# Kernel tuning notes

Hardware: AMD Instinct MI355X
Metric: run time of the kernel (lower is better)

## Reference

```python
import jax, jax.numpy as jnp
import numpy as np

N = 50000      # nodes
E = 800000     # edges (before self-loops)
NFEAT = 128
NHID = 32
H = 8
NCLASS = 47
NEG_SLOPE = 0.2  # PyG GATv2Conv default


def gatv2_layer(x, src, dst, Wl, Wr, att, b, n):
    """One GATv2Conv layer (concat over heads). att: [H, C]."""
    h, c = att.shape
    xl = (x @ Wl).reshape(n, h, c)  # source transform (lin_l)
    xr = (x @ Wr).reshape(n, h, c)  # target transform (lin_r)
    e = jax.nn.leaky_relu(xl[src] + xr[dst], NEG_SLOPE)   # [E, H, C]
    logits = jnp.einsum('ehc,hc->eh', e, att)             # [E, H]
    # segment softmax over incoming edges of each target node
    m = jax.ops.segment_max(logits, dst, num_segments=n)  # [N, H]
    alpha = jnp.exp(logits - m[dst])
    denom = jax.ops.segment_sum(alpha, dst, num_segments=n)
    alpha = alpha / (denom[dst] + 1e-16)
    msg = xl[src] * alpha[:, :, None]                     # [E, H, C]
    out = jax.ops.segment_sum(msg, dst, num_segments=n)   # [N, H, C]
    return out.reshape(n, h * c) + b


def setup_inputs():
    key = jax.random.key(0)
    ks = jax.random.split(key, 16)
    s = 0.1
    x = jax.random.normal(ks[0], (N, NFEAT), jnp.float32)
    edge_index = jax.random.randint(ks[1], (2, E), 0, N)
    HID = H * NHID  # 256
    params = dict(
        Wl0=jax.random.normal(ks[2], (NFEAT, HID), jnp.float32) * s,
        Wr0=jax.random.normal(ks[3], (NFEAT, HID), jnp.float32) * s,
        a0=jax.random.normal(ks[4], (H, NHID), jnp.float32) * s,
        b0=jnp.zeros((HID,), jnp.float32),
        Wl1=jax.random.normal(ks[5], (HID, HID), jnp.float32) * s,
        Wr1=jax.random.normal(ks[6], (HID, HID), jnp.float32) * s,
        a1=jax.random.normal(ks[7], (H, NHID), jnp.float32) * s,
        b1=jnp.zeros((HID,), jnp.float32),
        Wl2=jax.random.normal(ks[8], (HID, NCLASS), jnp.float32) * s,
        Wr2=jax.random.normal(ks[9], (HID, NCLASS), jnp.float32) * s,
        a2=jax.random.normal(ks[10], (1, NCLASS), jnp.float32) * s,
        b2=jnp.zeros((NCLASS,), jnp.float32),
    )
    return {"x": x, "edge_index": edge_index, **params}


def reference(x, edge_index, Wl0, Wr0, a0, b0, Wl1, Wr1, a1, b1, Wl2, Wr2, a2, b2):
    n = x.shape[0]
    # PyG GATv2Conv adds self-loops by default
    loops = jnp.arange(n, dtype=edge_index.dtype)
    src = jnp.concatenate([edge_index[0], loops])
    dst = jnp.concatenate([edge_index[1], loops])
    h = gatv2_layer(x, src, dst, Wl0, Wr0, a0, b0, n)
    h = jax.nn.elu(h)
    h = gatv2_layer(h, src, dst, Wl1, Wr1, a1, b1, n)
    h = jax.nn.elu(h)
    h = gatv2_layer(h, src, dst, Wl2, Wr2, a2, b2, n)
    return jax.nn.log_softmax(h, axis=-1)
```

## Files before the change

### kernel.cpp

```cpp
#include <hip/hip_runtime.h>
#include <cmath>


#define NFEAT 128
#define HID 256
#define NCLS 47
#define L2PAD 64
#define LOG2E 1.44269504088896340736f

typedef __attribute__((ext_vector_type(8))) short bf16x8;
typedef __attribute__((ext_vector_type(4))) float f32x4;
typedef __attribute__((ext_vector_type(2))) float f32x2;

__device__ __forceinline__ unsigned short f2b(float f) {
  unsigned int u = __builtin_bit_cast(unsigned int, f);
  u += 0x7FFFu + ((u >> 16) & 1u);
  return (unsigned short)(u >> 16);
}
__device__ __forceinline__ float b2f(unsigned short s) {
  return __builtin_bit_cast(float, (unsigned int)s << 16);
}
__device__ __forceinline__ f32x2 b2f2(unsigned int u) {
  return (f32x2){__builtin_bit_cast(float, u << 16),
                 __builtin_bit_cast(float, u & 0xFFFF0000u)};
}
__device__ __forceinline__ void glds16(const unsigned short* g, unsigned short* l) {
  __builtin_amdgcn_global_load_lds(
      (const __attribute__((address_space(1))) unsigned int*)g,
      (__attribute__((address_space(3))) unsigned int*)l, 16, 0, 0);
}

__global__ void k_cast_bf16(const float* __restrict__ in,
                            unsigned short* __restrict__ out, int n4) {
  int i = blockIdx.x * blockDim.x + threadIdx.x;
  if (i < n4) {
    float4 v = reinterpret_cast<const float4*>(in)[i];
    ushort4 o = {f2b(v.x), f2b(v.y), f2b(v.z), f2b(v.w)};
    reinterpret_cast<ushort4*>(out)[i] = o;
  }
}

struct WtArgs {
  const float* W[6];
  unsigned short* WT[6];
  int K[6], M[6], off[6], total;
  const float* att;
  float* att48;
};
__global__ void k_wt_all(WtArgs a) {
  int i = blockIdx.x * blockDim.x + threadIdx.x;
  if (i >= a.total) {
    int j = i - a.total;
    if (j < 48) a.att48[j] = (j < NCLS) ? a.att[j] * LOG2E : 0.f;
    return;
  }
  int s = 0;
  #pragma unroll
  for (int j = 1; j < 6; ++j) if (i >= a.off[j]) s = j;
  int jj = i - a.off[s];
  int K = a.K[s], M = a.M[s];
  int m = jj / K, k = jj - m * K;
  a.WT[s][jj] = (m < M) ? f2b(a.W[s][(size_t)k * M + m]) : (unsigned short)0;
}

__global__ void k_init_deg(int* __restrict__ deg, int n) {
  int i = blockIdx.x * blockDim.x + threadIdx.x;
  if (i < n) deg[i] = 1;
}

__global__ void k_count(const int* __restrict__ dst, int* __restrict__ deg, int e) {
  int i = blockIdx.x * blockDim.x + threadIdx.x;
  if (i < e) atomicAdd(&deg[dst[i]], 1);
}

__global__ __launch_bounds__(256) void k_bsum(const int* __restrict__ deg,
                                              int* __restrict__ bsum, int n) {
  int t = threadIdx.x;
  int base = blockIdx.x * 1024 + t * 4;
  int s = 0;
  if (base + 3 < n) {
    int4 v = *reinterpret_cast<const int4*>(deg + base);
    s = v.x + v.y + v.z + v.w;
  } else {
    for (int j = 0; j < 4; ++j) { int i = base + j; if (i < n) s += deg[i]; }
  }
  #pragma unroll
  for (int off = 1; off < 64; off <<= 1) s += __shfl_xor(s, off, 64);
  __shared__ int wsum[4];
  if ((t & 63) == 0) wsum[t >> 6] = s;
  __syncthreads();
  if (t == 0) bsum[blockIdx.x] = wsum[0] + wsum[1] + wsum[2] + wsum[3];
}

__global__ void k_scanb(int* __restrict__ bsum, int nb) {
  int lane = threadIdx.x;
  int v = (lane < nb) ? bsum[lane] : 0;
  #pragma unroll
  for (int off = 1; off < 64; off <<= 1) {
    int u = __shfl_up(v, off, 64);
    if (lane >= off) v += u;
  }
  if (lane < nb) bsum[lane] = v;
}

__global__ __launch_bounds__(256) void k_scanfinal(const int* __restrict__ deg,
                                                   const int* __restrict__ bscan,
                                                   int* __restrict__ rowptr,
                                                   int* __restrict__ adj,
                                                   int* __restrict__ vdst,
                                                   int* __restrict__ cursor, int n) {
  int t = threadIdx.x, b = blockIdx.x;
  int base = b * 1024 + t * 4;
  int v0 = 0, v1 = 0, v2 = 0, v3 = 0;
  if (base + 3 < n) {
    int4 v = *reinterpret_cast<const int4*>(deg + base);
    v0 = v.x; v1 = v.y; v2 = v.z; v3 = v.w;
  } else {
    if (base < n) v0 = deg[base];
    if (base + 1 < n) v1 = deg[base + 1];
    if (base + 2 < n) v2 = deg[base + 2];
    if (base + 3 < n) v3 = deg[base + 3];
  }
  int s = v0 + v1 + v2 + v3;
  int incl = s;
  #pragma unroll
  for (int off = 1; off < 64; off <<= 1) {
    int u = __shfl_up(incl, off, 64);
    if ((t & 63) >= off) incl += u;
  }
  __shared__ int wsum[4];
  int w = t >> 6, l = t & 63;
  if (l == 63) wsum[w] = incl;
  __syncthreads();
  int woff = 0;
  for (int j = 0; j < w; ++j) woff += wsum[j];
  int excl = incl - s + woff;
  int boff = (b == 0) ? 0 : bscan[b - 1];
  int p0 = boff + excl;
  int p1 = p0 + v0, p2 = p1 + v1, p3 = p2 + v2, p4 = p3 + v3;
  if (base < n)     { rowptr[base + 1] = p1; adj[p0] = base;     vdst[p0] = base;     cursor[base]     = p0 + 1; }
  if (base + 1 < n) { rowptr[base + 2] = p2; adj[p1] = base + 1; vdst[p1] = base + 1; cursor[base + 1] = p1 + 1; }
  if (base + 2 < n) { rowptr[base + 3] = p3; adj[p2] = base + 2; vdst[p2] = base + 2; cursor[base + 2] = p2 + 1; }
  if (base + 3 < n) { rowptr[base + 4] = p4; adj[p3] = base + 3; vdst[p3] = base + 3; cursor[base + 3] = p3 + 1; }
  if (b == 0 && t == 0) rowptr[0] = 0;
}

__global__ void k_scatter(const int* __restrict__ src, const int* __restrict__ dst,
                          int* __restrict__ cursor, int* __restrict__ adj,
                          int* __restrict__ vdst, int e) {
  int i = blockIdx.x * blockDim.x + threadIdx.x;
  if (i < e) {
    int d = dst[i];
    int p = atomicAdd(&cursor[d], 1);
    adj[p] = src[i];
    vdst[p] = d;
  }
}

__global__ __launch_bounds__(512) void gemm_dual_bf16_128(
    const unsigned short* __restrict__ X, const unsigned short* __restrict__ WlT,
    const unsigned short* __restrict__ WrT, unsigned short* __restrict__ XL,
    unsigned short* __restrict__ XR, int N, int K, int Mpad) {
  __shared__ __align__(16) unsigned short S[3 * 128 * 64];
  unsigned short* Xs = S;
  unsigned short* Ls = S + 8192;
  unsigned short* Rs = S + 16384;

  const int t = threadIdx.x;
  const int col0 = blockIdx.x * 128;
  const int row0 = blockIdx.y * 128;
  const int w = t >> 6, lane = t & 63;
  const int wr = w >> 2, wc = w & 3;
  const int r15 = lane & 15, kc = lane >> 4;
  const bool tail = (row0 + 128 > N);

  const int row_a = t >> 3,          c16_a = t & 7;
  const int row_b = (t + 512) >> 3,  c16_b = t & 7;
  const int sg_a = (c16_a ^ (row_a & 7)) * 8;
  const int sg_b = (c16_b ^ (row_b & 7)) * 8;
  unsigned short* d0 = S + w * 512;
  unsigned short* d1 = S + 4096 + w * 512;

  f32x4 accL[4][2], accR[4][2];
  #pragma unroll
  for (int rf = 0; rf < 4; ++rf)
    #pragma unroll
    for (int cf = 0; cf < 2; ++cf) {
      accL[rf][cf] = (f32x4){0.f, 0.f, 0.f, 0.f};
      accR[rf][cf] = (f32x4){0.f, 0.f, 0.f, 0.f};
    }

  for (int k0 = 0; k0 < K; k0 += 64) {
    glds16(WlT + (size_t)(col0 + row_a) * K + k0 + sg_a, d0 + 8192);
    glds16(WlT + (size_t)(col0 + row_b) * K + k0 + sg_b, d1 + 8192);
    glds16(WrT + (size_t)(col0 + row_a) * K + k0 + sg_a, d0 + 16384);
    glds16(WrT + (size_t)(col0 + row_b) * K + k0 + sg_b, d1 + 16384);
    if (!tail) {
      glds16(X + (size_t)(row0 + row_a) * K + k0 + sg_a, d0);
      glds16(X + (size_t)(row0 + row_b) * K + k0 + sg_b, d1);
    } else {
      uint4 va = (uint4){0, 0, 0, 0}, vb = (uint4){0, 0, 0, 0};
      if (row0 + row_a < N)
        va = *reinterpret_cast<const uint4*>(X + (size_t)(row0 + row_a) * K + k0 + sg_a);
      if (row0 + row_b < N)
        vb = *reinterpret_cast<const uint4*>(X + (size_t)(row0 + row_b) * K + k0 + sg_b);
      *reinterpret_cast<uint4*>(Xs + row_a * 64 + c16_a * 8) = va;
      *reinterpret_cast<uint4*>(Xs + row_b * 64 + c16_b * 8) = vb;
    }
    __syncthreads();

    #pragma unroll
    for (int ks = 0; ks < 2; ++ks) {
      const int c16 = ks * 4 + kc;
      bf16x8 a[4];
      #pragma unroll
      for (int rf = 0; rf < 4; ++rf) {
        const int rA = wr * 64 + rf * 16 + r15;
        a[rf] = *reinterpret_cast<const bf16x8*>(Xs + rA * 64 + ((c16 ^ (rA & 7)) * 8));
      }
      #pragma unroll
      for (int cf = 0; cf < 2; ++cf) {
        const int rB = wc * 32 + cf * 16 + r15;
        const int so = rB * 64 + ((c16 ^ (rB & 7)) * 8);
        const bf16x8 bl = *reinterpret_cast<const bf16x8*>(Ls + so);
        const bf16x8 br = *reinterpret_cast<const bf16x8*>(Rs + so);
        #pragma unroll
        for (int rf = 0; rf < 4; ++rf) {
          accL[rf][cf] = __builtin_amdgcn_mfma_f32_16x16x32_bf16(a[rf], bl, accL[rf][cf], 0, 0, 0);
          accR[rf][cf] = __builtin_amdgcn_mfma_f32_16x16x32_bf16(a[rf], br, accR[rf][cf], 0, 0, 0);
        }
      }
    }
    __syncthreads();
  }

  #pragma unroll
  for (int rf = 0; rf < 4; ++rf) {
    #pragma unroll
    for (int cf = 0; cf < 2; ++cf) {
      int cc = col0 + wc * 32 + cf * 16 + r15;
      #pragma unroll
      for (int i = 0; i < 4; ++i) {
        int rr = row0 + wr * 64 + rf * 16 + kc * 4 + i;
        if (rr < N) {
          XL[(size_t)rr * Mpad + cc] = f2b(accL[rf][cf][i]);
          XR[(size_t)rr * Mpad + cc] = f2b(accR[rf][cf][i]);
        }
      }
    }
  }
}

__global__ __launch_bounds__(256) void gemm_dual_bf16(
    const unsigned short* __restrict__ X, const unsigned short* __restrict__ WlT,
    const unsigned short* __restrict__ WrT, unsigned short* __restrict__ XL,
    unsigned short* __restrict__ XR, int N, int K, int Mpad) {
  __shared__ __align__(16) unsigned short S[3 * 64 * 64];
  unsigned short* Xs = S;
  unsigned short* Ls = S + 4096;
  unsigned short* Rs = S + 8192;

  const int t = threadIdx.x;
  const int col0 = blockIdx.x * 64;
  const int row0 = blockIdx.y * 64;
  const int w = t >> 6, lane = t & 63;
  const int r15 = lane & 15, kc = lane >> 4;
  const bool tail = (row0 + 64 > N);

  const int rowa = t >> 3, c16a = t & 7;
  const int rowb = (t + 256) >> 3, c16b = t & 7;
  const int sga = (c16a ^ (rowa & 7)) * 8;
  const int sgb = (c16b ^ (rowb & 7)) * 8;
  unsigned short* ldst0 = S + (w * 512);
  unsigned short* ldst1 = S + (2048 + w * 512);

  f32x4 accL[4], accR[4];
  #pragma unroll
  for (int i = 0; i < 4; ++i) {
    accL[i] = (f32x4){0.f, 0.f, 0.f, 0.f};
    accR[i] = (f32x4){0.f, 0.f, 0.f, 0.f};
  }

  const int rA = 16 * w + r15;

  for (int k0 = 0; k0 < K; k0 += 64) {
    glds16(WlT + (size_t)(col0 + rowa) * K + k0 + sga, ldst0 + 4096);
    glds16(WlT + (size_t)(col0 + rowb) * K + k0 + sgb, ldst1 + 4096);
    glds16(WrT + (size_t)(col0 + rowa) * K + k0 + sga, ldst0 + 8192);
    glds16(WrT + (size_t)(col0 + rowb) * K + k0 + sgb, ldst1 + 8192);
    if (!tail) {
      glds16(X + (size_t)(row0 + rowa) * K + k0 + sga, ldst0);
      glds16(X + (size_t)(row0 + rowb) * K + k0 + sgb, ldst1);
    } else {
      uint4 va = (uint4){0, 0, 0, 0}, vb = (uint4){0, 0, 0, 0};
      if (row0 + rowa < N)
        va = *reinterpret_cast<const uint4*>(X + (size_t)(row0 + rowa) * K + k0 + sga);
      if (row0 + rowb < N)
        vb = *reinterpret_cast<const uint4*>(X + (size_t)(row0 + rowb) * K + k0 + sgb);
      *reinterpret_cast<uint4*>(Xs + rowa * 64 + c16a * 8) = va;
      *reinterpret_cast<uint4*>(Xs + rowb * 64 + c16b * 8) = vb;
    }
    __syncthreads();

    #pragma unroll
    for (int ks = 0; ks < 2; ++ks) {
      const int c16 = ks * 4 + kc;
      const bf16x8 a = *reinterpret_cast<const bf16x8*>(
          Xs + rA * 64 + ((c16 ^ (rA & 7)) * 8));
      #pragma unroll
      for (int nf = 0; nf < 4; ++nf) {
        const int rB = nf * 16 + r15;
        const int so = rB * 64 + ((c16 ^ (rB & 7)) * 8);
        const bf16x8 bl = *reinterpret_cast<const bf16x8*>(Ls + so);
        const bf16x8 br = *reinterpret_cast<const bf16x8*>(Rs + so);
        accL[nf] = __builtin_amdgcn_mfma_f32_16x16x32_bf16(a, bl, accL[nf], 0, 0, 0);
        accR[nf] = __builtin_amdgcn_mfma_f32_16x16x32_bf16(a, br, accR[nf], 0, 0, 0);
      }
    }
    __syncthreads();
  }

  #pragma unroll
  for (int nf = 0; nf < 4; ++nf) {
    int cc = col0 + nf * 16 + r15;
    #pragma unroll
    for (int i = 0; i < 4; ++i) {
      int rr = row0 + 16 * w + kc * 4 + i;
      if (rr < N) {
        XL[(size_t)rr * Mpad + cc] = f2b(accL[nf][i]);
        XR[(size_t)rr * Mpad + cc] = f2b(accR[nf][i]);
      }
    }
  }
}

__global__ __launch_bounds__(256) void gat_node_hc(
    const unsigned short* __restrict__ xl, const unsigned short* __restrict__ xr,
    const float* __restrict__ att, const float* __restrict__ bias,
    const int* __restrict__ rowptr, const int* __restrict__ adj,
    unsigned short* __restrict__ out, int n) {
  int wid = (blockIdx.x * blockDim.x + threadIdx.x) >> 6;
  int lane = threadIdx.x & 63;
  if (wid >= n) return;
  const int q = lane & 31, half = lane >> 5;

  const uint4 xrp = *reinterpret_cast<const uint4*>(xr + (size_t)wid * HID + q * 8);
  const f32x2 xr2[4] = {b2f2(xrp.x), b2f2(xrp.y), b2f2(xrp.z), b2f2(xrp.w)};
  const float4 af0 = *reinterpret_cast<const float4*>(att + q * 8);
  const float4 af1 = *reinterpret_cast<const float4*>(att + q * 8 + 4);
  const f32x2 a2[4] = {{af0.x * LOG2E, af0.y * LOG2E}, {af0.z * LOG2E, af0.w * LOG2E},
                       {af1.x * LOG2E, af1.y * LOG2E}, {af1.z * LOG2E, af1.w * LOG2E}};

  float m = -1e30f, denom = 0.f;
  f32x2 acc[4] = {{0.f, 0.f}, {0.f, 0.f}, {0.f, 0.f}, {0.f, 0.f}};

  const int beg = rowptr[wid], end = rowptr[wid + 1];
  for (int base = beg; base < end; base += 2) {
    const int i = base + half;
    const bool act = i < end;
    const int u = adj[act ? i : base];
    const uint4 p = *reinterpret_cast<const uint4*>(xl + (size_t)u * HID + q * 8);
    const f32x2 x2[4] = {b2f2(p.x), b2f2(p.y), b2f2(p.z), b2f2(p.w)};
    f32x2 s2 = {0.f, 0.f};
    #pragma unroll
    for (int j = 0; j < 4; ++j) {
      f32x2 z = x2[j] + xr2[j];
      f32x2 lz = 0.2f * z;
      f32x2 r = {fmaxf(z.x, lz.x), fmaxf(z.y, lz.y)};
      s2 += r * a2[j];
    }
    float part = s2.x + s2.y;
    part += __shfl_xor(part, 1, 64);
    part += __shfl_xor(part, 2, 64);
    if (!act) part = -1e30f;
    if (__any(part > m + 11.54f)) {
      float mn = fmaxf(m, part);
      float so = exp2f(m - mn);
      float wn = act ? exp2f(part - mn) : 0.f;
      denom = denom * so + wn;
      #pragma unroll
      for (int j = 0; j < 4; ++j) acc[j] = acc[j] * so + wn * x2[j];
      m = mn;
    } else {
      float wn = act ? exp2f(part - m) : 0.f;
      denom += wn;
      #pragma unroll
      for (int j = 0; j < 4; ++j) acc[j] += wn * x2[j];
    }
  }

  float mo = __shfl_xor(m, 32, 64);
  float ms = fmaxf(m, mo);
  float sc = exp2f(m - ms);
  denom *= sc;
  denom += __shfl_xor(denom, 32, 64);
  #pragma unroll
  for (int j = 0; j < 4; ++j) {
    acc[j] *= sc;
    acc[j].x += __shfl_xor(acc[j].x, 32, 64);
    acc[j].y += __shfl_xor(acc[j].y, 32, 64);
  }

  if (half == 0) {
    const float inv = 1.f / (denom + 1e-16f);
    const float4 bf0 = *reinterpret_cast<const float4*>(bias + q * 8);
    const float4 bf1 = *reinterpret_cast<const float4*>(bias + q * 8 + 4);
    float o[8] = {acc[0].x * inv + bf0.x, acc[0].y * inv + bf0.y,
                  acc[1].x * inv + bf0.z, acc[1].y * inv + bf0.w,
                  acc[2].x * inv + bf1.x, acc[2].y * inv + bf1.y,
                  acc[3].x * inv + bf1.z, acc[3].y * inv + bf1.w};
    #pragma unroll
    for (int j = 0; j < 8; ++j) o[j] = o[j] > 0.f ? o[j] : (__expf(o[j]) - 1.f);
    uint4 ov;
    ov.x = (unsigned)f2b(o[0]) | ((unsigned)f2b(o[1]) << 16);
    ov.y = (unsigned)f2b(o[2]) | ((unsigned)f2b(o[3]) << 16);
    ov.z = (unsigned)f2b(o[4]) | ((unsigned)f2b(o[5]) << 16);
    ov.w = (unsigned)f2b(o[6]) | ((unsigned)f2b(o[7]) << 16);
    *reinterpret_cast<uint4*>(out + (size_t)wid * HID + q * 8) = ov;
  }
}

__global__ __launch_bounds__(256) void k_logit_l2(
    const unsigned short* __restrict__ xl, const unsigned short* __restrict__ xr,
    const float* __restrict__ att48, const int* __restrict__ adj,
    const int* __restrict__ vdst, float* __restrict__ logit, int total) {
  int i = blockIdx.x * blockDim.x + threadIdx.x;
  if (i >= total) return;
  const int u = adj[i], v = vdst[i];
  const uint4* pu = reinterpret_cast<const uint4*>(xl + (size_t)u * L2PAD);
  const uint4* pv = reinterpret_cast<const uint4*>(xr + (size_t)v * L2PAD);
  f32x2 s2 = {0.f, 0.f};
  #pragma unroll
  for (int b = 0; b < 6; ++b) {
    const uint4 xu = pu[b], xv = pv[b];
    const f32x2* a2 = reinterpret_cast<const f32x2*>(att48 + b * 8);
    const unsigned ua[4] = {xu.x, xu.y, xu.z, xu.w};
    const unsigned va[4] = {xv.x, xv.y, xv.z, xv.w};
    #pragma unroll
    for (int j = 0; j < 4; ++j) {
      f32x2 z = b2f2(ua[j]) + b2f2(va[j]);
      f32x2 lz = 0.2f * z;
      f32x2 r = {fmaxf(z.x, lz.x), fmaxf(z.y, lz.y)};
      s2 += r * a2[j];
    }
  }
  logit[i] = s2.x + s2.y;
}

__global__ __launch_bounds__(256) void gat_node_l2(
    const unsigned short* __restrict__ xl, const float* __restrict__ logit,
    const float* __restrict__ bias, const int* __restrict__ rowptr,
    const int* __restrict__ adj, float* __restrict__ out, int n) {
  int wid = (blockIdx.x * blockDim.x + threadIdx.x) >> 6;
  int lane = threadIdx.x & 63;
  if (wid >= n) return;
  const bool act = lane < NCLS;
  const int beg = rowptr[wid], end = rowptr[wid + 1];

  float mx = -1e30f;
  for (int i = beg + lane; i < end; i += 64) mx = fmaxf(mx, logit[i]);
  #pragma unroll
  for (int off = 1; off < 64; off <<= 1) mx = fmaxf(mx, __shfl_xor(mx, off, 64));

  float denom = 0.f, acc = 0.f;
  int i = beg;
  for (; i + 1 < end; i += 2) {
    int u0 = adj[i], u1 = adj[i + 1];
    float w0 = exp2f(logit[i] - mx);
    float w1 = exp2f(logit[i + 1] - mx);
    float x0 = act ? b2f(xl[(size_t)u0 * L2PAD + lane]) : 0.f;
    float x1 = act ? b2f(xl[(size_t)u1 * L2PAD + lane]) : 0.f;
    denom += w0 + w1;
    acc += w0 * x0 + w1 * x1;
  }
  if (i < end) {
    int u0 = adj[i];
    float w0 = exp2f(logit[i] - mx);
    float x0 = act ? b2f(xl[(size_t)u0 * L2PAD + lane]) : 0.f;
    denom += w0;
    acc += w0 * x0;
  }

  float r = acc / (denom + 1e-16f) + (act ? bias[lane] : 0.f);
  float rm = act ? r : -1e30f;
  #pragma unroll
  for (int off = 1; off < 64; off <<= 1) rm = fmaxf(rm, __shfl_xor(rm, off, 64));
  float se = act ? __expf(r - rm) : 0.f;
  #pragma unroll
  for (int off = 1; off < 64; off <<= 1) se += __shfl_xor(se, off, 64);
  if (act) out[(size_t)wid * NCLS + lane] = r - rm - __logf(se);
}

extern "C" void kernel_launch(void* const* d_in, const int* in_sizes, int n_in,
                              void* d_out, int out_size, void* d_ws, size_t ws_size,
                              hipStream_t stream) {
  const float* x   = (const float*)d_in[0];
  const int* ei    = (const int*)d_in[1];
  const float* Wl0 = (const float*)d_in[2];
  const float* Wr0 = (const float*)d_in[3];
  const float* a0  = (const float*)d_in[4];
  const float* b0  = (const float*)d_in[5];
  const float* Wl1 = (const float*)d_in[6];
  const float* Wr1 = (const float*)d_in[7];
  const float* a1  = (const float*)d_in[8];
  const float* b1  = (const float*)d_in[9];
  const float* Wl2 = (const float*)d_in[10];
  const float* Wr2 = (const float*)d_in[11];
  const float* a2  = (const float*)d_in[12];
  const float* b2  = (const float*)d_in[13];

  const int N = in_sizes[0] / NFEAT;
  const int E = in_sizes[1] / 2;
  const int* src = ei;
  const int* dst = ei + E;
  const int total = E + N;

  char* ws = (char*)d_ws;
  unsigned short* xlb = (unsigned short*)ws; ws += (size_t)N * HID * 2;
  unsigned short* xrb = (unsigned short*)ws; ws += (size_t)N * HID * 2;
  unsigned short* xb  = (unsigned short*)ws; ws += (size_t)N * HID * 2;
  unsigned short* hb  = (unsigned short*)ws; ws += (size_t)N * HID * 2;
  unsigned short* WT  = (unsigned short*)ws; ws += (size_t)6 * HID * HID * 2;
  float* logit = (float*)ws; ws += (size_t)total * sizeof(float);
  float* att48 = (float*)ws; ws += 64 * sizeof(float);
  int* deg    = (int*)ws; ws += (size_t)N * sizeof(int);
  int* rowptr = (int*)ws; ws += (size_t)(N + 8) * sizeof(int);
  int* bsum   = (int*)ws; ws += (size_t)64 * sizeof(int);
  int* adj    = (int*)ws; ws += (size_t)total * sizeof(int);
  int* vdst   = (int*)ws; ws += (size_t)total * sizeof(int);

  unsigned short* WlT0 = WT + 0 * HID * HID;
  unsigned short* WrT0 = WT + 1 * HID * HID;
  unsigned short* WlT1 = WT + 2 * HID * HID;
  unsigned short* WrT1 = WT + 3 * HID * HID;
  unsigned short* WlT2 = WT + 4 * HID * HID;
  unsigned short* WrT2 = WT + 5 * HID * HID;

  const int TB = 256;
  const int nbScan = (N + 1023) / 1024;

  k_cast_bf16<<<(N * NFEAT / 4 + TB - 1) / TB, TB, 0, stream>>>(x, xb, N * NFEAT / 4);
  {
    WtArgs a;
    const float* Wsrc[6] = {Wl0, Wr0, Wl1, Wr1, Wl2, Wr2};
    unsigned short* Wdst[6] = {WlT0, WrT0, WlT1, WrT1, WlT2, WrT2};
    int Ks[6] = {NFEAT, NFEAT, HID, HID, HID, HID};
    int Ms[6] = {HID, HID, HID, HID, NCLS, NCLS};
    int Mp[6] = {HID, HID, HID, HID, L2PAD, L2PAD};
    int off = 0;
    for (int s = 0; s < 6; ++s) {
      a.W[s] = Wsrc[s]; a.WT[s] = Wdst[s]; a.K[s] = Ks[s]; a.M[s] = Ms[s];
      a.off[s] = off; off += Mp[s] * Ks[s];
    }
    a.total = off;
    a.att = a2; a.att48 = att48;
    k_wt_all<<<(a.total + 48 + TB - 1) / TB, TB, 0, stream>>>(a);
  }

  k_init_deg<<<(N + TB - 1) / TB, TB, 0, stream>>>(deg, N);
  k_count<<<(E + TB - 1) / TB, TB, 0, stream>>>(dst, deg, E);
  k_bsum<<<nbScan, TB, 0, stream>>>(deg, bsum, N);
  k_scanb<<<1, 64, 0, stream>>>(bsum, nbScan);
  k_scanfinal<<<nbScan, TB, 0, stream>>>(deg, bsum, rowptr, adj, vdst, deg, N);
  k_scatter<<<(E + TB - 1) / TB, TB, 0, stream>>>(src, dst, deg, adj, vdst, E);

  const int nodeBlocks = (N + 3) / 4;
  const int rb128 = (N + 127) / 128;
  const int rb64 = (N + 63) / 64;

  {
    dim3 g(HID / 128, rb128);
    gemm_dual_bf16_128<<<g, 512, 0, stream>>>(xb, WlT0, WrT0, xlb, xrb, N, NFEAT, HID);
    gat_node_hc<<<nodeBlocks, 256, 0, stream>>>(xlb, xrb, a0, b0, rowptr, adj, hb, N);
  }
  {
    dim3 g(HID / 128, rb128);
    gemm_dual_bf16_128<<<g, 512, 0, stream>>>(hb, WlT1, WrT1, xlb, xrb, N, HID, HID);
    gat_node_hc<<<nodeBlocks, 256, 0, stream>>>(xlb, xrb, a1, b1, rowptr, adj, xb, N);
  }
  {
    dim3 g(1, rb64);
    gemm_dual_bf16<<<g, 256, 0, stream>>>(xb, WlT2, WrT2, xlb, xrb, N, HID, L2PAD);
    k_logit_l2<<<(total + TB - 1) / TB, TB, 0, stream>>>(xlb, xrb, att48, adj,
                                                         vdst, logit, total);
    gat_node_l2<<<nodeBlocks, 256, 0, stream>>>(xlb, logit, b2, rowptr, adj,
                                                (float*)d_out, N);
  }
}
```

Baseline: 431.9 us.

## Prefetch next neighbor row, fuse degree init, use natural exp, enlarge node blocks

Software-pipelines the gather in the per-node attention kernel by loading the next edge's source row before processing the current one, to hide gather latency. It also folds degree initialization into the bf16 cast kernel to drop a launch, and switches from exp2 with LOG2E-scaled attention to __expf, with a lower rescale threshold. Node kernels now use 1024-thread blocks covering 16 nodes each. The prefetch adds registers, and the larger blocks may change occupancy.

```diff
diff --git a/kernel.cpp b/kernel.cpp
--- a/kernel.cpp
+++ b/kernel.cpp
@@ -31,12 +31,16 @@
 }
 
 __global__ void k_cast_bf16(const float* __restrict__ in,
-                            unsigned short* __restrict__ out, int n4) {
+                            unsigned short* __restrict__ out, int n4,
+                            int* __restrict__ deg, int n) {
   int i = blockIdx.x * blockDim.x + threadIdx.x;
   if (i < n4) {
     float4 v = reinterpret_cast<const float4*>(in)[i];
     ushort4 o = {f2b(v.x), f2b(v.y), f2b(v.z), f2b(v.w)};
     reinterpret_cast<ushort4*>(out)[i] = o;
+  } else {
+    int j = i - n4;
+    if (j < n) deg[j] = 1;
   }
 }
 
@@ -61,11 +65,6 @@
   int K = a.K[s], M = a.M[s];
   int m = jj / K, k = jj - m * K;
   a.WT[s][jj] = (m < M) ? f2b(a.W[s][(size_t)k * M + m]) : (unsigned short)0;
-}
-
-__global__ void k_init_deg(int* __restrict__ deg, int n) {
-  int i = blockIdx.x * blockDim.x + threadIdx.x;
-  if (i < n) deg[i] = 1;
 }
 
 __global__ void k_count(const int* __restrict__ dst, int* __restrict__ deg, int e) {
@@ -334,7 +333,7 @@
   }
 }
 
-__global__ __launch_bounds__(256) void gat_node_hc(
+__global__ __launch_bounds__(1024) void gat_node_hc(
     const unsigned short* __restrict__ xl, const unsigned short* __restrict__ xr,
     const float* __restrict__ att, const float* __restrict__ bias,
     const int* __restrict__ rowptr, const int* __restrict__ adj,
@@ -348,18 +347,24 @@
   const f32x2 xr2[4] = {b2f2(xrp.x), b2f2(xrp.y), b2f2(xrp.z), b2f2(xrp.w)};
   const float4 af0 = *reinterpret_cast<const float4*>(att + q * 8);
   const float4 af1 = *reinterpret_cast<const float4*>(att + q * 8 + 4);
-  const f32x2 a2[4] = {{af0.x * LOG2E, af0.y * LOG2E}, {af0.z * LOG2E, af0.w * LOG2E},
-                       {af1.x * LOG2E, af1.y * LOG2E}, {af1.z * LOG2E, af1.w * LOG2E}};
+  const f32x2 a2[4] = {{af0.x, af0.y}, {af0.z, af0.w},
+                       {af1.x, af1.y}, {af1.z, af1.w}};
 
   float m = -1e30f, denom = 0.f;
   f32x2 acc[4] = {{0.f, 0.f}, {0.f, 0.f}, {0.f, 0.f}, {0.f, 0.f}};
 
   const int beg = rowptr[wid], end = rowptr[wid + 1];
+  int i = beg + half;
+  bool act = i < end;
+  int u = adj[act ? i : beg];
+  uint4 p = *reinterpret_cast<const uint4*>(xl + (size_t)u * HID + q * 8);
+
   for (int base = beg; base < end; base += 2) {
-    const int i = base + half;
-    const bool act = i < end;
-    const int u = adj[act ? i : base];
-    const uint4 p = *reinterpret_cast<const uint4*>(xl + (size_t)u * HID + q * 8);
+    const int i2 = base + 2 + half;
+    const bool act2 = i2 < end;
+    const int u2 = adj[act2 ? i2 : beg];
+    const uint4 p2 = *reinterpret_cast<const uint4*>(xl + (size_t)u2 * HID + q * 8);
+
     const f32x2 x2[4] = {b2f2(p.x), b2f2(p.y), b2f2(p.z), b2f2(p.w)};
     f32x2 s2 = {0.f, 0.f};
     #pragma unroll
@@ -373,25 +378,27 @@
     part += __shfl_xor(part, 1, 64);
     part += __shfl_xor(part, 2, 64);
     if (!act) part = -1e30f;
-    if (__any(part > m + 11.54f)) {
+    if (__any(part > m + 8.f)) {
       float mn = fmaxf(m, part);
-      float so = exp2f(m - mn);
-      float wn = act ? exp2f(part - mn) : 0.f;
+      float so = __expf(m - mn);
+      float wn = act ? __expf(part - mn) : 0.f;
       denom = denom * so + wn;
       #pragma unroll
       for (int j = 0; j < 4; ++j) acc[j] = acc[j] * so + wn * x2[j];
       m = mn;
     } else {
-      float wn = act ? exp2f(part - m) : 0.f;
+      float wn = act ? __expf(part - m) : 0.f;
       denom += wn;
       #pragma unroll
       for (int j = 0; j < 4; ++j) acc[j] += wn * x2[j];
     }
+    p = p2;
+    act = act2;
   }
 
   float mo = __shfl_xor(m, 32, 64);
   float ms = fmaxf(m, mo);
-  float sc = exp2f(m - ms);
+  float sc = __expf(m - ms);
   denom *= sc;
   denom += __shfl_xor(denom, 32, 64);
   #pragma unroll
@@ -447,7 +454,7 @@
   logit[i] = s2.x + s2.y;
 }
 
-__global__ __launch_bounds__(256) void gat_node_l2(
+__global__ __launch_bounds__(1024) void gat_node_l2(
     const unsigned short* __restrict__ xl, const float* __restrict__ logit,
     const float* __restrict__ bias, const int* __restrict__ rowptr,
     const int* __restrict__ adj, float* __restrict__ out, int n) {
@@ -538,8 +545,9 @@
 
   const int TB = 256;
   const int nbScan = (N + 1023) / 1024;
-
-  k_cast_bf16<<<(N * NFEAT / 4 + TB - 1) / TB, TB, 0, stream>>>(x, xb, N * NFEAT / 4);
+  const int n4 = N * NFEAT / 4;
+
+  k_cast_bf16<<<(n4 + N + TB - 1) / TB, TB, 0, stream>>>(x, xb, n4, deg, N);
   {
     WtArgs a;
     const float* Wsrc[6] = {Wl0, Wr0, Wl1, Wr1, Wl2, Wr2};
@@ -557,33 +565,32 @@
     k_wt_all<<<(a.total + 48 + TB - 1) / TB, TB, 0, stream>>>(a);
   }
 
-  k_init_deg<<<(N + TB - 1) / TB, TB, 0, stream>>>(deg, N);
   k_count<<<(E + TB - 1) / TB, TB, 0, stream>>>(dst, deg, E);
   k_bsum<<<nbScan, TB, 0, stream>>>(deg, bsum, N);
   k_scanb<<<1, 64, 0, stream>>>(bsum, nbScan);
   k_scanfinal<<<nbScan, TB, 0, stream>>>(deg, bsum, rowptr, adj, vdst, deg, N);
   k_scatter<<<(E + TB - 1) / TB, TB, 0, stream>>>(src, dst, deg, adj, vdst, E);
 
-  const int nodeBlocks = (N + 3) / 4;
+  const int nodeBlocks = (N + 15) / 16;
   const int rb128 = (N + 127) / 128;
   const int rb64 = (N + 63) / 64;
 
   {
     dim3 g(HID / 128, rb128);
     gemm_dual_bf16_128<<<g, 512, 0, stream>>>(xb, WlT0, WrT0, xlb, xrb, N, NFEAT, HID);
-    gat_node_hc<<<nodeBlocks, 256, 0, stream>>>(xlb, xrb, a0, b0, rowptr, adj, hb, N);
+    gat_node_hc<<<nodeBlocks, 1024, 0, stream>>>(xlb, xrb, a0, b0, rowptr, adj, hb, N);
   }
   {
     dim3 g(HID / 128, rb128);
     gemm_dual_bf16_128<<<g, 512, 0, stream>>>(hb, WlT1, WrT1, xlb, xrb, N, HID, HID);
-    gat_node_hc<<<nodeBlocks, 256, 0, stream>>>(xlb, xrb, a1, b1, rowptr, adj, xb, N);
+    gat_node_hc<<<nodeBlocks, 1024, 0, stream>>>(xlb, xrb, a1, b1, rowptr, adj, xb, N);
   }
   {
     dim3 g(1, rb64);
     gemm_dual_bf16<<<g, 256, 0, stream>>>(xb, WlT2, WrT2, xlb, xrb, N, HID, L2PAD);
     k_logit_l2<<<(total + TB - 1) / TB, TB, 0, stream>>>(xlb, xrb, att48, adj,
                                                          vdst, logit, total);
-    gat_node_l2<<<nodeBlocks, 256, 0, stream>>>(xlb, logit, b2, rowptr, adj,
-                                                (float*)d_out, N);
-  }
-}
+    gat_node_l2<<<nodeBlocks, 1024, 0, stream>>>(xlb, logit, b2, rowptr, adj,
+                                                 (float*)d_out, N);
+  }
+}
```

Result: slower. 448.7 us (+3.9%).
